# Optimization experiments

Measured on AMD Instinct MI355X. Metric: run time of the kernel, lower is better.

The kernel has to match this reference:

```python
import jax, jax.numpy as jnp
import numpy as np

ALPHA = 0.2  # leaky relu negative slope
W_SIZE = 128  # window_size


def setup_inputs() -> dict:
    key = jax.random.key(0)
    ks = jax.random.split(key, 5)
    B, W, K, E = 4, 128, 256, 256  # E = 2*W (gatv2 doubles embed_dim)
    return {
        "x": jax.random.normal(ks[0], (B, W, K), dtype=jnp.float32),
        "lin_w": jax.random.normal(ks[1], (E, 2 * W), dtype=jnp.float32) * (1.0 / np.sqrt(2 * W)),
        "lin_b": jax.random.normal(ks[2], (E,), dtype=jnp.float32) * 0.02,
        "a_vec": jax.random.normal(ks[3], (E,), dtype=jnp.float32) * (1.414 / np.sqrt(E)),
        "bias": jax.random.normal(ks[4], (K, K), dtype=jnp.float32) * 0.02,
    }


def reference(x, lin_w, lin_b, a_vec, bias):
    # x: (B, W, K) -> v: (B, K, W), one W-length vector per node
    v = jnp.transpose(x, (0, 2, 1))
    # GATv2: lin(concat(v_i, v_j)) decomposed: concat @ lin_w.T = v_i @ W1.T + v_j @ W2.T
    W1 = lin_w[:, :W_SIZE]  # (E, W) applied to the repeated (source) block
    W2 = lin_w[:, W_SIZE:]  # (E, W) applied to the alternating (target) block
    u = jnp.einsum("bkw,ew->bke", v, W1)                 # (B, K, E)
    t = jnp.einsum("bkw,ew->bke", v, W2) + lin_b          # (B, K, E)
    pre = u[:, :, None, :] + t[:, None, :, :]             # (B, K, K, E) pairwise
    act = jax.nn.leaky_relu(pre, negative_slope=ALPHA)
    e = jnp.einsum("bije,e->bij", act, a_vec)             # (B, K, K)
    e = e + bias
    attn = jax.nn.softmax(e, axis=-1)
    h = jax.nn.sigmoid(jnp.einsum("bij,bjw->biw", attn, v))  # (B, K, W)
    return jnp.transpose(h, (0, 2, 1))  # (B, W, K)
```

## Files before the change

kernel.cpp:

```cpp
#include <hip/hip_runtime.h>
#include <math.h>

#define NB 4
#define WDIM 128
#define KDIM 256
#define EDIM 256

__device__ __forceinline__ float dot4(float4 a, float4 b) {
    return a.x * b.x + a.y * b.y + a.z * b.z + a.w * b.w;
}

__global__ __launch_bounds__(256) void k_ut5(const float* __restrict__ x,
                                             const float* __restrict__ lin_w,
                                             const float* __restrict__ lin_b,
                                             float* __restrict__ u_ws,
                                             float* __restrict__ t_ws) {
    __shared__ float vrow[8 * WDIM];
    const int blk = blockIdx.x;
    const int b  = blk >> 7;
    const int kt = (blk >> 2) & 31;
    const int eq = blk & 3;
    const int k0 = kt * 8;
    const int tid = threadIdx.x;
    const int e  = eq * 64 + (tid & 63);
    const int ks = tid >> 6;

    if (tid < WDIM) {
        const float* xp = x + ((size_t)b * WDIM + tid) * KDIM + k0;
        float4 v0 = *(const float4*)xp;
        float4 v1 = *(const float4*)(xp + 4);
        vrow[0 * WDIM + tid] = v0.x; vrow[1 * WDIM + tid] = v0.y;
        vrow[2 * WDIM + tid] = v0.z; vrow[3 * WDIM + tid] = v0.w;
        vrow[4 * WDIM + tid] = v1.x; vrow[5 * WDIM + tid] = v1.y;
        vrow[6 * WDIM + tid] = v1.z; vrow[7 * WDIM + tid] = v1.w;
    }
    __syncthreads();

    const float4* wr = (const float4*)(lin_w + (size_t)e * 2 * WDIM);
    float u0 = 0.f, u1 = 0.f, t0 = 0.f, t1 = 0.f;
#pragma unroll 8
    for (int q = 0; q < 32; ++q) {
        float4 w1 = wr[q];
        float4 w2 = wr[32 + q];
        float4 va = *(const float4*)&vrow[(ks * 2 + 0) * WDIM + q * 4];
        float4 vb = *(const float4*)&vrow[(ks * 2 + 1) * WDIM + q * 4];
        u0 += dot4(w1, va); u1 += dot4(w1, vb);
        t0 += dot4(w2, va); t1 += dot4(w2, vb);
    }
    const float lb = lin_b[e];
    const int k = k0 + ks * 2;
    const size_t o0 = ((size_t)b * KDIM + k) * EDIM + e;
    u_ws[o0] = u0;         u_ws[o0 + EDIM] = u1;
    t_ws[o0] = t0 + lb;    t_ws[o0 + EDIM] = t1 + lb;
}

__global__ __launch_bounds__(256, 4) void k_e5(const float* __restrict__ a_vec,
                                               const float* __restrict__ bias,
                                               const float* __restrict__ u_ws,
                                               const float* __restrict__ t_ws,
                                               float* __restrict__ e_ws) {
    __shared__ float a2_lds[EDIM];
    const int blk = blockIdx.x;
    const int b  = blk >> 8;
    const int it = (blk >> 3) & 31;
    const int jt = blk & 7;
    const int i0 = it * 8;
    const int j0 = jt * 32;
    const int tid  = threadIdx.x;
    const int wv   = tid >> 6;
    const int lane = tid & 63;
    const int s  = lane & 7;
    const int jj = lane >> 3;
    const int iA = i0 + wv * 2;

    if (tid < 64) {
        float4 av = *(const float4*)(a_vec + tid * 4);
        *(float4*)&a2_lds[tid * 4] =
            make_float4(0.4f * av.x, 0.4f * av.y, 0.4f * av.z, 0.4f * av.w);
    }

    const float* uAp = u_ws + ((size_t)b * KDIM + iA) * EDIM;
    float4 uA[8], uB[8];
#pragma unroll
    for (int q = 0; q < 8; ++q) {
        uA[q] = *(const float4*)(uAp + q * 32 + s * 4);
        uB[q] = *(const float4*)(uAp + EDIM + q * 32 + s * 4);
    }
    __syncthreads();

    float ruA = 0.f, ruB = 0.f;
#pragma unroll
    for (int q = 0; q < 8; ++q) {
        float4 a2 = *(const float4*)&a2_lds[q * 32 + s * 4];
        ruA += dot4(a2, uA[q]);
        ruB += dot4(a2, uB[q]);
    }

    const float* tb = t_ws + (size_t)b * KDIM * EDIM;
#pragma unroll
    for (int jg = 0; jg < 4; ++jg) {
        const int j = j0 + jg * 8 + jj;
        const float* tr = tb + (size_t)j * EDIM;
        float4 tld[8];
#pragma unroll
        for (int q = 0; q < 8; ++q) tld[q] = *(const float4*)(tr + q * 32 + s * 4);

        float accA = 0.f, accB = 0.f, rt = 0.f;
#pragma unroll
        for (int q = 0; q < 8; ++q) {
            float4 a2 = *(const float4*)&a2_lds[q * 32 + s * 4];
            float4 t4 = tld[q];
            rt += dot4(a2, t4);
            accA += a2.x * fabsf(uA[q].x + t4.x) + a2.y * fabsf(uA[q].y + t4.y)
                  + a2.z * fabsf(uA[q].z + t4.z) + a2.w * fabsf(uA[q].w + t4.w);
            accB += a2.x * fabsf(uB[q].x + t4.x) + a2.y * fabsf(uB[q].y + t4.y)
                  + a2.z * fabsf(uB[q].z + t4.z) + a2.w * fabsf(uB[q].w + t4.w);
        }
        float zA = accA + 1.5f * (ruA + rt);
        float zB = accB + 1.5f * (ruB + rt);
        zA += __shfl_xor(zA, 1, 64); zB += __shfl_xor(zB, 1, 64);
        zA += __shfl_xor(zA, 2, 64); zB += __shfl_xor(zB, 2, 64);
        zA += __shfl_xor(zA, 4, 64); zB += __shfl_xor(zB, 4, 64);
        if (s == 0) {
            e_ws[((size_t)b * KDIM + iA) * KDIM + j]     = zA + bias[(size_t)iA * KDIM + j];
            e_ws[((size_t)b * KDIM + iA + 1) * KDIM + j] = zB + bias[(size_t)(iA + 1) * KDIM + j];
        }
    }
}

__global__ __launch_bounds__(256) void k_sh5(const float* __restrict__ x,
                                             const float* __restrict__ e_ws,
                                             float* __restrict__ out) {
    __shared__ float attn_lds[4][260];
    const int blk = blockIdx.x;
    const int b  = blk >> 8;
    const int it = (blk >> 2) & 63;
    const int wq = blk & 3;
    const int i0 = it * 4;
    const int w0 = wq * 32;
    const int tid  = threadIdx.x;
    const int wv   = tid >> 6;
    const int lane = tid & 63;

    {
        float4 ev = *(const float4*)(e_ws + ((size_t)b * KDIM + i0 + wv) * KDIM + lane * 4);
        float m = fmaxf(fmaxf(ev.x, ev.y), fmaxf(ev.z, ev.w));
#pragma unroll
        for (int o = 1; o < 64; o <<= 1) m = fmaxf(m, __shfl_xor(m, o, 64));
        float4 p;
        p.x = __expf(ev.x - m); p.y = __expf(ev.y - m);
        p.z = __expf(ev.z - m); p.w = __expf(ev.w - m);
        float ssum = p.x + p.y + p.z + p.w;
#pragma unroll
        for (int o = 1; o < 64; o <<= 1) ssum += __shfl_xor(ssum, o, 64);
        const float inv = 1.0f / ssum;
        p.x *= inv; p.y *= inv; p.z *= inv; p.w *= inv;
        *(float4*)&attn_lds[wv][lane * 4] = p;
    }
    __syncthreads();

    const int s  = lane & 7;
    const int ww = lane >> 3;
    const int w  = w0 + wv * 8 + ww;
    const float* xr = x + ((size_t)b * WDIM + w) * KDIM;
    float acc[4] = {0.f, 0.f, 0.f, 0.f};
#pragma unroll
    for (int q = 0; q < 8; ++q) {
        float4 x4 = *(const float4*)(xr + q * 32 + s * 4);
#pragma unroll
        for (int i = 0; i < 4; ++i) {
            float4 at = *(const float4*)&attn_lds[i][q * 32 + s * 4];
            acc[i] += dot4(at, x4);
        }
    }
#pragma unroll
    for (int i = 0; i < 4; ++i) {
        acc[i] += __shfl_xor(acc[i], 1, 64);
        acc[i] += __shfl_xor(acc[i], 2, 64);
        acc[i] += __shfl_xor(acc[i], 4, 64);
    }
    if (s == 0) {
        float4 o;
        o.x = 1.f / (1.f + __expf(-acc[0]));
        o.y = 1.f / (1.f + __expf(-acc[1]));
        o.z = 1.f / (1.f + __expf(-acc[2]));
        o.w = 1.f / (1.f + __expf(-acc[3]));
        *(float4*)(out + ((size_t)b * WDIM + w) * KDIM + i0) = o;
    }
}

extern "C" void kernel_launch(void* const* d_in, const int* in_sizes, int n_in,
                              void* d_out, int out_size, void* d_ws, size_t ws_size,
                              hipStream_t stream) {
    (void)in_sizes; (void)n_in; (void)out_size; (void)ws_size;
    const float* x     = (const float*)d_in[0];
    const float* lin_w = (const float*)d_in[1];
    const float* lin_b = (const float*)d_in[2];
    const float* a_vec = (const float*)d_in[3];
    const float* bias  = (const float*)d_in[4];
    float* out = (float*)d_out;

    float* u_ws = (float*)d_ws;
    float* t_ws = u_ws + (size_t)NB * KDIM * EDIM;
    float* e_ws = t_ws + (size_t)NB * KDIM * EDIM;

    k_ut5<<<512, 256, 0, stream>>>(x, lin_w, lin_b, u_ws, t_ws);
    k_e5<<<1024, 256, 0, stream>>>(a_vec, bias, u_ws, t_ws, e_ws);
    k_sh5<<<1024, 256, 0, stream>>>(x, e_ws, out);
}
```

Before: 36.88 us.

## Restructure pairwise score kernel to stage u rows in LDS and hold t in registers

The e-kernel now gives each thread one j column with its t row kept in registers, and stages the block's 8 u rows in shared memory so every wave reads all eight i rows from LDS. Previously each wave kept two u rows in registers and looped over four j groups, reloading t from global memory each time. The scaled a_vec is loaded into registers instead of LDS, and the ru terms are reduced once per block and passed through shared memory. The new layout adds LDS read traffic and an extra barrier, and the occupancy hint in launch_bounds is dropped.

Result: faster. 35.92 us (-2.6%).

```diff
diff --git a/kernel.cpp b/kernel.cpp
--- a/kernel.cpp
+++ b/kernel.cpp
@@ -10,7 +10,7 @@
     return a.x * b.x + a.y * b.y + a.z * b.z + a.w * b.w;
 }
 
-__global__ __launch_bounds__(256) void k_ut5(const float* __restrict__ x,
+__global__ __launch_bounds__(256) void k_ut6(const float* __restrict__ x,
                                              const float* __restrict__ lin_w,
                                              const float* __restrict__ lin_b,
                                              float* __restrict__ u_ws,
@@ -54,12 +54,13 @@
     t_ws[o0] = t0 + lb;    t_ws[o0 + EDIM] = t1 + lb;
 }
 
-__global__ __launch_bounds__(256, 4) void k_e5(const float* __restrict__ a_vec,
-                                               const float* __restrict__ bias,
-                                               const float* __restrict__ u_ws,
-                                               const float* __restrict__ t_ws,
-                                               float* __restrict__ e_ws) {
-    __shared__ float a2_lds[EDIM];
+__global__ __launch_bounds__(256) void k_e6(const float* __restrict__ a_vec,
+                                            const float* __restrict__ bias,
+                                            const float* __restrict__ u_ws,
+                                            const float* __restrict__ t_ws,
+                                            float* __restrict__ e_ws) {
+    __shared__ float u_lds[8 * 256];
+    __shared__ float ru_lds[8];
     const int blk = blockIdx.x;
     const int b  = blk >> 8;
     const int it = (blk >> 3) & 31;
@@ -71,64 +72,85 @@
     const int lane = tid & 63;
     const int s  = lane & 7;
     const int jj = lane >> 3;
-    const int iA = i0 + wv * 2;
-
-    if (tid < 64) {
-        float4 av = *(const float4*)(a_vec + tid * 4);
-        *(float4*)&a2_lds[tid * 4] =
-            make_float4(0.4f * av.x, 0.4f * av.y, 0.4f * av.z, 0.4f * av.w);
-    }
-
-    const float* uAp = u_ws + ((size_t)b * KDIM + iA) * EDIM;
-    float4 uA[8], uB[8];
+    const int j  = j0 + wv * 8 + jj;
+
+    const float* tr = t_ws + ((size_t)b * KDIM + j) * EDIM;
+    float4 tld[8];
+#pragma unroll
+    for (int q = 0; q < 8; ++q) tld[q] = *(const float4*)(tr + q * 32 + s * 4);
+
+    float4 a2[8];
 #pragma unroll
     for (int q = 0; q < 8; ++q) {
-        uA[q] = *(const float4*)(uAp + q * 32 + s * 4);
-        uB[q] = *(const float4*)(uAp + EDIM + q * 32 + s * 4);
-    }
-    __syncthreads();
-
-    float ruA = 0.f, ruB = 0.f;
-#pragma unroll
-    for (int q = 0; q < 8; ++q) {
-        float4 a2 = *(const float4*)&a2_lds[q * 32 + s * 4];
-        ruA += dot4(a2, uA[q]);
-        ruB += dot4(a2, uB[q]);
-    }
-
-    const float* tb = t_ws + (size_t)b * KDIM * EDIM;
-#pragma unroll
-    for (int jg = 0; jg < 4; ++jg) {
-        const int j = j0 + jg * 8 + jj;
-        const float* tr = tb + (size_t)j * EDIM;
-        float4 tld[8];
-#pragma unroll
-        for (int q = 0; q < 8; ++q) tld[q] = *(const float4*)(tr + q * 32 + s * 4);
-
-        float accA = 0.f, accB = 0.f, rt = 0.f;
+        float4 av = *(const float4*)(a_vec + q * 32 + s * 4);
+        a2[q] = make_float4(0.4f * av.x, 0.4f * av.y, 0.4f * av.z, 0.4f * av.w);
+    }
+
+    {
+        const int r = tid >> 5;
+        const int c = (tid & 31) * 4;
+        const float* up = u_ws + ((size_t)b * KDIM + i0 + r) * EDIM;
+        *(float4*)&u_lds[r * 256 + c]       = *(const float4*)(up + c);
+        *(float4*)&u_lds[r * 256 + c + 128] = *(const float4*)(up + c + 128);
+    }
+    __syncthreads();
+
+    float rt = 0.f;
+#pragma unroll
+    for (int q = 0; q < 8; ++q) rt += dot4(a2[q], tld[q]);
+
+    {
+        float r0 = 0.f, r1 = 0.f;
 #pragma unroll
         for (int q = 0; q < 8; ++q) {
-            float4 a2 = *(const float4*)&a2_lds[q * 32 + s * 4];
+            float4 ua = *(const float4*)&u_lds[(2 * wv) * 256 + q * 32 + s * 4];
+            float4 ub = *(const float4*)&u_lds[(2 * wv + 1) * 256 + q * 32 + s * 4];
+            r0 += dot4(a2[q], ua);
+            r1 += dot4(a2[q], ub);
+        }
+        r0 += __shfl_xor(r0, 1, 64); r1 += __shfl_xor(r1, 1, 64);
+        r0 += __shfl_xor(r0, 2, 64); r1 += __shfl_xor(r1, 2, 64);
+        r0 += __shfl_xor(r0, 4, 64); r1 += __shfl_xor(r1, 4, 64);
+        if (lane == 0) { ru_lds[2 * wv] = r0; ru_lds[2 * wv + 1] = r1; }
+    }
+    __syncthreads();
+
+    float acc[8];
+#pragma unroll
+    for (int i = 0; i < 8; ++i) acc[i] = 0.f;
+#pragma unroll
+    for (int i = 0; i < 8; ++i) {
+        float a = 0.f;
+#pragma unroll
+        for (int q = 0; q < 8; ++q) {
+            float4 u4 = *(const float4*)&u_lds[i * 256 + q * 32 + s * 4];
             float4 t4 = tld[q];
-            rt += dot4(a2, t4);
-            accA += a2.x * fabsf(uA[q].x + t4.x) + a2.y * fabsf(uA[q].y + t4.y)
-                  + a2.z * fabsf(uA[q].z + t4.z) + a2.w * fabsf(uA[q].w + t4.w);
-            accB += a2.x * fabsf(uB[q].x + t4.x) + a2.y * fabsf(uB[q].y + t4.y)
-                  + a2.z * fabsf(uB[q].z + t4.z) + a2.w * fabsf(uB[q].w + t4.w);
-        }
-        float zA = accA + 1.5f * (ruA + rt);
-        float zB = accB + 1.5f * (ruB + rt);
-        zA += __shfl_xor(zA, 1, 64); zB += __shfl_xor(zB, 1, 64);
-        zA += __shfl_xor(zA, 2, 64); zB += __shfl_xor(zB, 2, 64);
-        zA += __shfl_xor(zA, 4, 64); zB += __shfl_xor(zB, 4, 64);
-        if (s == 0) {
-            e_ws[((size_t)b * KDIM + iA) * KDIM + j]     = zA + bias[(size_t)iA * KDIM + j];
-            e_ws[((size_t)b * KDIM + iA + 1) * KDIM + j] = zB + bias[(size_t)(iA + 1) * KDIM + j];
-        }
-    }
-}
-
-__global__ __launch_bounds__(256) void k_sh5(const float* __restrict__ x,
+            a += a2[q].x * fabsf(u4.x + t4.x) + a2[q].y * fabsf(u4.y + t4.y)
+               + a2[q].z * fabsf(u4.z + t4.z) + a2[q].w * fabsf(u4.w + t4.w);
+        }
+        acc[i] = a;
+    }
+
+#pragma unroll
+    for (int i = 0; i < 8; ++i) {
+        float z = acc[i] + 1.5f * rt;
+        z += __shfl_xor(z, 1, 64);
+        z += __shfl_xor(z, 2, 64);
+        z += __shfl_xor(z, 4, 64);
+        acc[i] = z;
+    }
+    if (s == 0) {
+        const float* brow = bias + j;
+        float* erow = e_ws + ((size_t)b * KDIM) * KDIM + j;
+#pragma unroll
+        for (int i = 0; i < 8; ++i) {
+            erow[(size_t)(i0 + i) * KDIM] =
+                acc[i] + 1.5f * ru_lds[i] + brow[(size_t)(i0 + i) * KDIM];
+        }
+    }
+}
+
+__global__ __launch_bounds__(256) void k_sh6(const float* __restrict__ x,
                                              const float* __restrict__ e_ws,
                                              float* __restrict__ out) {
     __shared__ float attn_lds[4][260];
@@ -204,7 +226,7 @@
     float* t_ws = u_ws + (size_t)NB * KDIM * EDIM;
     float* e_ws = t_ws + (size_t)NB * KDIM * EDIM;
 
-    k_ut5<<<512, 256, 0, stream>>>(x, lin_w, lin_b, u_ws, t_ws);
-    k_e5<<<1024, 256, 0, stream>>>(a_vec, bias, u_ws, t_ws, e_ws);
-    k_sh5<<<1024, 256, 0, stream>>>(x, e_ws, out);
-}
+    k_ut6<<<512, 256, 0, stream>>>(x, lin_w, lin_b, u_ws, t_ws);
+    k_e6<<<1024, 256, 0, stream>>>(a_vec, bias, u_ws, t_ws, e_ws);
+    k_sh6<<<1024, 256, 0, stream>>>(x, e_ws, out);
+}
```

## Transpose t to E-major and split pairwise score over E quarters

Applied to the files above, without the earlier changes.

The projection kernel now writes t transposed (E-major) through an LDS staging tile, so the pairwise kernel can have each lane own four j columns and read t coalesced without any cross-lane shuffle reduction. The score kernel splits E into four quarters per block and writes partial sums to four planes. The softmax kernel then adds the planes, the row term from u, and the bias. This removes the shuffle reductions and the LDS a-vector staging, at the cost of extra workspace traffic (four partial planes) and a per-row reduction in the softmax kernel.

Result: slower. 44.59 us (+20.9%).

```diff
diff --git a/kernel.cpp b/kernel.cpp
--- a/kernel.cpp
+++ b/kernel.cpp
@@ -10,20 +10,22 @@
     return a.x * b.x + a.y * b.y + a.z * b.z + a.w * b.w;
 }
 
-__global__ __launch_bounds__(256) void k_ut5(const float* __restrict__ x,
+__global__ __launch_bounds__(256) void k_ut7(const float* __restrict__ x,
                                              const float* __restrict__ lin_w,
                                              const float* __restrict__ lin_b,
                                              float* __restrict__ u_ws,
-                                             float* __restrict__ t_ws) {
+                                             float* __restrict__ tT_ws) {
     __shared__ float vrow[8 * WDIM];
+    __shared__ float t_lds[64][9];
     const int blk = blockIdx.x;
     const int b  = blk >> 7;
     const int kt = (blk >> 2) & 31;
     const int eq = blk & 3;
     const int k0 = kt * 8;
     const int tid = threadIdx.x;
-    const int e  = eq * 64 + (tid & 63);
-    const int ks = tid >> 6;
+    const int el  = tid & 63;
+    const int e   = eq * 64 + el;
+    const int ks  = tid >> 6;
 
     if (tid < WDIM) {
         const float* xp = x + ((size_t)b * WDIM + tid) * KDIM + k0;
@@ -50,86 +52,67 @@
     const float lb = lin_b[e];
     const int k = k0 + ks * 2;
     const size_t o0 = ((size_t)b * KDIM + k) * EDIM + e;
-    u_ws[o0] = u0;         u_ws[o0 + EDIM] = u1;
-    t_ws[o0] = t0 + lb;    t_ws[o0 + EDIM] = t1 + lb;
-}
-
-__global__ __launch_bounds__(256, 4) void k_e5(const float* __restrict__ a_vec,
-                                               const float* __restrict__ bias,
-                                               const float* __restrict__ u_ws,
-                                               const float* __restrict__ t_ws,
-                                               float* __restrict__ e_ws) {
-    __shared__ float a2_lds[EDIM];
+    u_ws[o0] = u0;  u_ws[o0 + EDIM] = u1;
+
+    t_lds[el][ks * 2 + 0] = t0 + lb;
+    t_lds[el][ks * 2 + 1] = t1 + lb;
+    __syncthreads();
+
+    const int e_w = tid >> 2;
+    const int c2  = (tid & 3) * 2;
+    float2 tv = make_float2(t_lds[e_w][c2], t_lds[e_w][c2 + 1]);
+    *(float2*)(tT_ws + ((size_t)b * EDIM + eq * 64 + e_w) * KDIM + k0 + c2) = tv;
+}
+
+__global__ __launch_bounds__(256) void k_e7(const float* __restrict__ a_vec,
+                                            const float* __restrict__ u_ws,
+                                            const float* __restrict__ tT_ws,
+                                            float* __restrict__ z_ws) {
     const int blk = blockIdx.x;
     const int b  = blk >> 8;
-    const int it = (blk >> 3) & 31;
-    const int jt = blk & 7;
-    const int i0 = it * 8;
-    const int j0 = jt * 32;
-    const int tid  = threadIdx.x;
-    const int wv   = tid >> 6;
-    const int lane = tid & 63;
-    const int s  = lane & 7;
-    const int jj = lane >> 3;
-    const int iA = i0 + wv * 2;
-
-    if (tid < 64) {
-        float4 av = *(const float4*)(a_vec + tid * 4);
-        *(float4*)&a2_lds[tid * 4] =
-            make_float4(0.4f * av.x, 0.4f * av.y, 0.4f * av.z, 0.4f * av.w);
-    }
-
-    const float* uAp = u_ws + ((size_t)b * KDIM + iA) * EDIM;
-    float4 uA[8], uB[8];
-#pragma unroll
-    for (int q = 0; q < 8; ++q) {
-        uA[q] = *(const float4*)(uAp + q * 32 + s * 4);
-        uB[q] = *(const float4*)(uAp + EDIM + q * 32 + s * 4);
-    }
-    __syncthreads();
-
-    float ruA = 0.f, ruB = 0.f;
-#pragma unroll
-    for (int q = 0; q < 8; ++q) {
-        float4 a2 = *(const float4*)&a2_lds[q * 32 + s * 4];
-        ruA += dot4(a2, uA[q]);
-        ruB += dot4(a2, uB[q]);
-    }
-
-    const float* tb = t_ws + (size_t)b * KDIM * EDIM;
-#pragma unroll
-    for (int jg = 0; jg < 4; ++jg) {
-        const int j = j0 + jg * 8 + jj;
-        const float* tr = tb + (size_t)j * EDIM;
-        float4 tld[8];
-#pragma unroll
-        for (int q = 0; q < 8; ++q) tld[q] = *(const float4*)(tr + q * 32 + s * 4);
-
-        float accA = 0.f, accB = 0.f, rt = 0.f;
-#pragma unroll
-        for (int q = 0; q < 8; ++q) {
-            float4 a2 = *(const float4*)&a2_lds[q * 32 + s * 4];
-            float4 t4 = tld[q];
-            rt += dot4(a2, t4);
-            accA += a2.x * fabsf(uA[q].x + t4.x) + a2.y * fabsf(uA[q].y + t4.y)
-                  + a2.z * fabsf(uA[q].z + t4.z) + a2.w * fabsf(uA[q].w + t4.w);
-            accB += a2.x * fabsf(uB[q].x + t4.x) + a2.y * fabsf(uB[q].y + t4.y)
-                  + a2.z * fabsf(uB[q].z + t4.z) + a2.w * fabsf(uB[q].w + t4.w);
+    const int it = (blk >> 2) & 63;
+    const int eh = blk & 3;
+    const int wv   = threadIdx.x >> 6;
+    const int lane = threadIdx.x & 63;
+    const int i  = it * 4 + wv;
+    const int e0 = eh * 64;
+
+    const float* urow  = u_ws + ((size_t)b * KDIM + i) * EDIM + e0;
+    const float* arow  = a_vec + e0;
+    const float* tbase = tT_ws + ((size_t)b * EDIM + e0) * KDIM + lane * 4;
+
+    float4 acc = make_float4(0.f, 0.f, 0.f, 0.f);
+    float4 rt  = make_float4(0.f, 0.f, 0.f, 0.f);
+
+#pragma unroll 4
+    for (int e4 = 0; e4 < 16; ++e4) {
+        float4 uv = *(const float4*)(urow + e4 * 4);
+        float4 av = *(const float4*)(arow + e4 * 4);
+        float uc[4] = {uv.x, uv.y, uv.z, uv.w};
+        float ac[4] = {av.x, av.y, av.z, av.w};
+#pragma unroll
+        for (int r = 0; r < 4; ++r) {
+            float4 t4 = *(const float4*)(tbase + (size_t)(e4 * 4 + r) * KDIM);
+            const float c = 0.4f * ac[r];
+            const float d = 0.6f * ac[r];
+            acc.x += c * fabsf(uc[r] + t4.x);  rt.x += d * t4.x;
+            acc.y += c * fabsf(uc[r] + t4.y);  rt.y += d * t4.y;
+            acc.z += c * fabsf(uc[r] + t4.z);  rt.z += d * t4.z;
+            acc.w += c * fabsf(uc[r] + t4.w);  rt.w += d * t4.w;
         }
-        float zA = accA + 1.5f * (ruA + rt);
-        float zB = accB + 1.5f * (ruB + rt);
-        zA += __shfl_xor(zA, 1, 64); zB += __shfl_xor(zB, 1, 64);
-        zA += __shfl_xor(zA, 2, 64); zB += __shfl_xor(zB, 2, 64);
-        zA += __shfl_xor(zA, 4, 64); zB += __shfl_xor(zB, 4, 64);
-        if (s == 0) {
-            e_ws[((size_t)b * KDIM + iA) * KDIM + j]     = zA + bias[(size_t)iA * KDIM + j];
-            e_ws[((size_t)b * KDIM + iA + 1) * KDIM + j] = zB + bias[(size_t)(iA + 1) * KDIM + j];
-        }
-    }
-}
-
-__global__ __launch_bounds__(256) void k_sh5(const float* __restrict__ x,
-                                             const float* __restrict__ e_ws,
+    }
+    float4 z;
+    z.x = acc.x + rt.x; z.y = acc.y + rt.y;
+    z.z = acc.z + rt.z; z.w = acc.w + rt.w;
+    *(float4*)(z_ws + (size_t)eh * (NB * KDIM * KDIM)
+                    + ((size_t)b * KDIM + i) * KDIM + lane * 4) = z;
+}
+
+__global__ __launch_bounds__(256) void k_sh7(const float* __restrict__ x,
+                                             const float* __restrict__ a_vec,
+                                             const float* __restrict__ bias,
+                                             const float* __restrict__ u_ws,
+                                             const float* __restrict__ z_ws,
                                              float* __restrict__ out) {
     __shared__ float attn_lds[4][260];
     const int blk = blockIdx.x;
@@ -141,9 +124,29 @@
     const int tid  = threadIdx.x;
     const int wv   = tid >> 6;
     const int lane = tid & 63;
+    const int i = i0 + wv;
 
     {
-        float4 ev = *(const float4*)(e_ws + ((size_t)b * KDIM + i0 + wv) * KDIM + lane * 4);
+        const size_t plane = (size_t)NB * KDIM * KDIM;
+        const size_t roff  = ((size_t)b * KDIM + i) * KDIM + lane * 4;
+        float4 z0 = *(const float4*)(z_ws + roff);
+        float4 z1 = *(const float4*)(z_ws + plane + roff);
+        float4 z2 = *(const float4*)(z_ws + 2 * plane + roff);
+        float4 z3 = *(const float4*)(z_ws + 3 * plane + roff);
+
+        float4 uv = *(const float4*)(u_ws + ((size_t)b * KDIM + i) * EDIM + lane * 4);
+        float4 av = *(const float4*)(a_vec + lane * 4);
+        float ru = 0.6f * dot4(av, uv);
+#pragma unroll
+        for (int o = 1; o < 64; o <<= 1) ru += __shfl_xor(ru, o, 64);
+
+        float4 bv = *(const float4*)(bias + (size_t)i * KDIM + lane * 4);
+        float4 ev;
+        ev.x = z0.x + z1.x + z2.x + z3.x + ru + bv.x;
+        ev.y = z0.y + z1.y + z2.y + z3.y + ru + bv.y;
+        ev.z = z0.z + z1.z + z2.z + z3.z + ru + bv.z;
+        ev.w = z0.w + z1.w + z2.w + z3.w + ru + bv.w;
+
         float m = fmaxf(fmaxf(ev.x, ev.y), fmaxf(ev.z, ev.w));
 #pragma unroll
         for (int o = 1; o < 64; o <<= 1) m = fmaxf(m, __shfl_xor(m, o, 64));
@@ -168,16 +171,16 @@
     for (int q = 0; q < 8; ++q) {
         float4 x4 = *(const float4*)(xr + q * 32 + s * 4);
 #pragma unroll
-        for (int i = 0; i < 4; ++i) {
-            float4 at = *(const float4*)&attn_lds[i][q * 32 + s * 4];
-            acc[i] += dot4(at, x4);
+        for (int ii = 0; ii < 4; ++ii) {
+            float4 at = *(const float4*)&attn_lds[ii][q * 32 + s * 4];
+            acc[ii] += dot4(at, x4);
         }
     }
 #pragma unroll
-    for (int i = 0; i < 4; ++i) {
-        acc[i] += __shfl_xor(acc[i], 1, 64);
-        acc[i] += __shfl_xor(acc[i], 2, 64);
-        acc[i] += __shfl_xor(acc[i], 4, 64);
+    for (int ii = 0; ii < 4; ++ii) {
+        acc[ii] += __shfl_xor(acc[ii], 1, 64);
+        acc[ii] += __shfl_xor(acc[ii], 2, 64);
+        acc[ii] += __shfl_xor(acc[ii], 4, 64);
     }
     if (s == 0) {
         float4 o;
@@ -200,11 +203,11 @@
     const float* bias  = (const float*)d_in[4];
     float* out = (float*)d_out;
 
-    float* u_ws = (float*)d_ws;
-    float* t_ws = u_ws + (size_t)NB * KDIM * EDIM;
-    float* e_ws = t_ws + (size_t)NB * KDIM * EDIM;
-
-    k_ut5<<<512, 256, 0, stream>>>(x, lin_w, lin_b, u_ws, t_ws);
-    k_e5<<<1024, 256, 0, stream>>>(a_vec, bias, u_ws, t_ws, e_ws);
-    k_sh5<<<1024, 256, 0, stream>>>(x, e_ws, out);
-}
+    float* u_ws  = (float*)d_ws;
+    float* tT_ws = u_ws + (size_t)NB * KDIM * EDIM;
+    float* z_ws  = tT_ws + (size_t)NB * KDIM * EDIM;
+
+    k_ut7<<<512, 256, 0, stream>>>(x, lin_w, lin_b, u_ws, tT_ws);
+    k_e7<<<1024, 256, 0, stream>>>(a_vec, u_ws, tT_ws, z_ws);
+    k_sh7<<<1024, 256, 0, stream>>>(x, a_vec, bias, u_ws, z_ws, out);
+}
```

## Remap blocks to XCDs per batch and restructure pairwise score kernel tiling

Applied to the files above, without the earlier changes.

All three kernels now remap block IDs so that each batch's blocks land on the same pair of XCDs, with the aim of keeping that batch's u/t/e working set in the local L2. The pairwise score kernel now keeps one target row t_j and a_vec in registers per thread. It streams 8 source rows u_i from global memory in two groups of four, instead of holding two u rows and looping over four j rows. The LDS staging of a_vec is dropped and the leaky-relu coefficients are applied after the reduction. This trades register-resident u reuse for repeated global/L2 loads of u, which are shared across threads in the same wave.

Result: slower. 41.48 us (+12.5%).

```diff
diff --git a/kernel.cpp b/kernel.cpp
--- a/kernel.cpp
+++ b/kernel.cpp
@@ -10,20 +10,22 @@
     return a.x * b.x + a.y * b.y + a.z * b.z + a.w * b.w;
 }
 
-__global__ __launch_bounds__(256) void k_ut5(const float* __restrict__ x,
-                                             const float* __restrict__ lin_w,
-                                             const float* __restrict__ lin_b,
-                                             float* __restrict__ u_ws,
-                                             float* __restrict__ t_ws) {
+
+__global__ __launch_bounds__(256) void k_ut11(const float* __restrict__ x,
+                                              const float* __restrict__ lin_w,
+                                              const float* __restrict__ lin_b,
+                                              float* __restrict__ u_ws,
+                                              float* __restrict__ t_ws) {
     __shared__ float vrow[8 * WDIM];
     const int blk = blockIdx.x;
-    const int b  = blk >> 7;
-    const int kt = (blk >> 2) & 31;
-    const int eq = blk & 3;
-    const int k0 = kt * 8;
+    const int xcd = blk & 7;
+    const int b   = xcd >> 1;
+    const int wid = ((blk >> 3) << 1) | (xcd & 1);
+    const int k0  = (wid >> 2) * 8;
+    const int eq  = wid & 3;
     const int tid = threadIdx.x;
-    const int e  = eq * 64 + (tid & 63);
-    const int ks = tid >> 6;
+    const int e   = eq * 64 + (tid & 63);
+    const int ks  = tid >> 6;
 
     if (tid < WDIM) {
         const float* xp = x + ((size_t)b * WDIM + tid) * KDIM + k0;
@@ -54,90 +56,83 @@
     t_ws[o0] = t0 + lb;    t_ws[o0 + EDIM] = t1 + lb;
 }
 
-__global__ __launch_bounds__(256, 4) void k_e5(const float* __restrict__ a_vec,
-                                               const float* __restrict__ bias,
-                                               const float* __restrict__ u_ws,
-                                               const float* __restrict__ t_ws,
-                                               float* __restrict__ e_ws) {
-    __shared__ float a2_lds[EDIM];
+__global__ __launch_bounds__(256) void k_e11(const float* __restrict__ a_vec,
+                                             const float* __restrict__ bias,
+                                             const float* __restrict__ u_ws,
+                                             const float* __restrict__ t_ws,
+                                             float* __restrict__ e_ws) {
     const int blk = blockIdx.x;
-    const int b  = blk >> 8;
-    const int it = (blk >> 3) & 31;
-    const int jt = blk & 7;
-    const int i0 = it * 8;
-    const int j0 = jt * 32;
+    const int xcd = blk & 7;
+    const int b   = xcd >> 1;
+    const int wid = ((blk >> 3) << 1) | (xcd & 1);
+    const int i0  = (wid >> 3) * 8;
+    const int jt  = wid & 7;
     const int tid  = threadIdx.x;
     const int wv   = tid >> 6;
     const int lane = tid & 63;
     const int s  = lane & 7;
     const int jj = lane >> 3;
-    const int iA = i0 + wv * 2;
-
-    if (tid < 64) {
-        float4 av = *(const float4*)(a_vec + tid * 4);
-        *(float4*)&a2_lds[tid * 4] =
-            make_float4(0.4f * av.x, 0.4f * av.y, 0.4f * av.z, 0.4f * av.w);
-    }
-
-    const float* uAp = u_ws + ((size_t)b * KDIM + iA) * EDIM;
-    float4 uA[8], uB[8];
-#pragma unroll
-    for (int q = 0; q < 8; ++q) {
-        uA[q] = *(const float4*)(uAp + q * 32 + s * 4);
-        uB[q] = *(const float4*)(uAp + EDIM + q * 32 + s * 4);
-    }
-    __syncthreads();
-
-    float ruA = 0.f, ruB = 0.f;
-#pragma unroll
-    for (int q = 0; q < 8; ++q) {
-        float4 a2 = *(const float4*)&a2_lds[q * 32 + s * 4];
-        ruA += dot4(a2, uA[q]);
-        ruB += dot4(a2, uB[q]);
-    }
-
-    const float* tb = t_ws + (size_t)b * KDIM * EDIM;
-#pragma unroll
-    for (int jg = 0; jg < 4; ++jg) {
-        const int j = j0 + jg * 8 + jj;
-        const float* tr = tb + (size_t)j * EDIM;
-        float4 tld[8];
-#pragma unroll
-        for (int q = 0; q < 8; ++q) tld[q] = *(const float4*)(tr + q * 32 + s * 4);
-
-        float accA = 0.f, accB = 0.f, rt = 0.f;
+    const int j  = jt * 32 + wv * 8 + jj;
+
+    const float* trp = t_ws + ((size_t)b * KDIM + j) * EDIM;
+    float4 tld[8];
+#pragma unroll
+    for (int q = 0; q < 8; ++q) tld[q] = *(const float4*)(trp + q * 32 + s * 4);
+
+    float4 av[8];
+#pragma unroll
+    for (int q = 0; q < 8; ++q) av[q] = *(const float4*)(a_vec + q * 32 + s * 4);
+
+    float rt = 0.f;
+#pragma unroll
+    for (int q = 0; q < 8; ++q) rt += dot4(av[q], tld[q]);
+    rt += __shfl_xor(rt, 1, 64);
+    rt += __shfl_xor(rt, 2, 64);
+    rt += __shfl_xor(rt, 4, 64);
+
+#pragma unroll
+    for (int p = 0; p < 2; ++p) {
+        const int ib = i0 + p * 4;
+        const float* up0 = u_ws + ((size_t)b * KDIM + ib) * EDIM;
+        float acc[4] = {0.f, 0.f, 0.f, 0.f};
+        float ru[4]  = {0.f, 0.f, 0.f, 0.f};
 #pragma unroll
         for (int q = 0; q < 8; ++q) {
-            float4 a2 = *(const float4*)&a2_lds[q * 32 + s * 4];
-            float4 t4 = tld[q];
-            rt += dot4(a2, t4);
-            accA += a2.x * fabsf(uA[q].x + t4.x) + a2.y * fabsf(uA[q].y + t4.y)
-                  + a2.z * fabsf(uA[q].z + t4.z) + a2.w * fabsf(uA[q].w + t4.w);
-            accB += a2.x * fabsf(uB[q].x + t4.x) + a2.y * fabsf(uB[q].y + t4.y)
-                  + a2.z * fabsf(uB[q].z + t4.z) + a2.w * fabsf(uB[q].w + t4.w);
+            const float4 aa = av[q];
+            const float4 t4 = tld[q];
+#pragma unroll
+            for (int i = 0; i < 4; ++i) {
+                float4 u4 = *(const float4*)(up0 + (size_t)i * EDIM + q * 32 + s * 4);
+                ru[i]  += dot4(aa, u4);
+                acc[i] += aa.x * fabsf(u4.x + t4.x) + aa.y * fabsf(u4.y + t4.y)
+                        + aa.z * fabsf(u4.z + t4.z) + aa.w * fabsf(u4.w + t4.w);
+            }
         }
-        float zA = accA + 1.5f * (ruA + rt);
-        float zB = accB + 1.5f * (ruB + rt);
-        zA += __shfl_xor(zA, 1, 64); zB += __shfl_xor(zB, 1, 64);
-        zA += __shfl_xor(zA, 2, 64); zB += __shfl_xor(zB, 2, 64);
-        zA += __shfl_xor(zA, 4, 64); zB += __shfl_xor(zB, 4, 64);
-        if (s == 0) {
-            e_ws[((size_t)b * KDIM + iA) * KDIM + j]     = zA + bias[(size_t)iA * KDIM + j];
-            e_ws[((size_t)b * KDIM + iA + 1) * KDIM + j] = zB + bias[(size_t)(iA + 1) * KDIM + j];
+#pragma unroll
+        for (int i = 0; i < 4; ++i) {
+            float z = 0.4f * acc[i] + 0.6f * ru[i];
+            z += __shfl_xor(z, 1, 64);
+            z += __shfl_xor(z, 2, 64);
+            z += __shfl_xor(z, 4, 64);
+            z += 0.6f * rt;
+            if (s == 0) {
+                e_ws[((size_t)b * KDIM + ib + i) * KDIM + j] =
+                    z + bias[(size_t)(ib + i) * KDIM + j];
+            }
         }
     }
 }
 
-__global__ __launch_bounds__(256) void k_sh5(const float* __restrict__ x,
-                                             const float* __restrict__ e_ws,
-                                             float* __restrict__ out) {
+__global__ __launch_bounds__(256) void k_sh11(const float* __restrict__ x,
+                                              const float* __restrict__ e_ws,
+                                              float* __restrict__ out) {
     __shared__ float attn_lds[4][260];
     const int blk = blockIdx.x;
-    const int b  = blk >> 8;
-    const int it = (blk >> 2) & 63;
-    const int wq = blk & 3;
-    const int i0 = it * 4;
-    const int w0 = wq * 32;
+    const int xcd = blk & 7;
+    const int b   = xcd >> 1;
+    const int wid = ((blk >> 3) << 1) | (xcd & 1);
+    const int i0  = (wid >> 2) * 4;
+    const int w0  = (wid & 3) * 32;
     const int tid  = threadIdx.x;
     const int wv   = tid >> 6;
     const int lane = tid & 63;
@@ -204,7 +199,7 @@
     float* t_ws = u_ws + (size_t)NB * KDIM * EDIM;
     float* e_ws = t_ws + (size_t)NB * KDIM * EDIM;
 
-    k_ut5<<<512, 256, 0, stream>>>(x, lin_w, lin_b, u_ws, t_ws);
-    k_e5<<<1024, 256, 0, stream>>>(a_vec, bias, u_ws, t_ws, e_ws);
-    k_sh5<<<1024, 256, 0, stream>>>(x, e_ws, out);
-}
+    k_ut11<<<512, 256, 0, stream>>>(x, lin_w, lin_b, u_ws, t_ws);
+    k_e11<<<1024, 256, 0, stream>>>(a_vec, bias, u_ws, t_ws, e_ws);
+    k_sh11<<<1024, 256, 0, stream>>>(x, e_ws, out);
+}
```
